# Kernel optimization log

Measured on AMD Instinct MI355X. Metric: run time of the kernel, lower is better.

Reference implementation:

```python
import jax, jax.numpy as jnp
import numpy as np

B, T, N, F_IN, F_OUT = 8, 64, 256, 128, 64
NEG_INF = -9e15


def setup_inputs() -> dict:
    key = jax.random.key(0)
    k_h, k_w, k_a, k_adj = jax.random.split(key, 4)
    h = jax.random.normal(k_h, (B, T, N, F_IN), dtype=jnp.float32)
    W = jax.random.normal(k_w, (F_IN, F_OUT), dtype=jnp.float32) * (1.414 / np.sqrt(F_IN))
    a = jax.random.normal(k_a, (2 * F_OUT, 1), dtype=jnp.float32) * 0.1
    # binary adjacency with guaranteed self-loops so every softmax row is valid
    adj = (jax.random.uniform(k_adj, (N, N)) > 0.5).astype(jnp.float32)
    adj = jnp.maximum(adj, jnp.eye(N, dtype=jnp.float32))
    return {"h": h, "W": W, "a": a, "adj": adj}


def reference(h, W, a, adj):
    # Wh: [B, T, N, F_OUT]
    Wh = jnp.einsum('btnf,fo->btno', h, W)
    a1 = a[:F_OUT, 0]   # [F_OUT]
    a2 = a[F_OUT:, 0]   # [F_OUT]
    Wh1 = jnp.einsum('btno,o->btn', Wh, a1)  # source scores
    Wh2 = jnp.einsum('btno,o->btn', Wh, a2)  # target scores
    # e: [B, T, N, N] = leakyrelu(Wh1_i + Wh2_j)
    e = jax.nn.leaky_relu(Wh1[..., :, None] + Wh2[..., None, :], negative_slope=0.01)
    attention = jnp.where(adj > 0, e, NEG_INF)
    alpha = jax.nn.softmax(attention, axis=-1)
    # dropout is identity at inference (training=False)
    h_prime = jnp.einsum('btnm,btmo->btno', alpha, Wh)
    return jax.nn.elu(h_prime)  # concat=True path
```

## Files before the change

### kernel.cpp

```cpp
#include <hip/hip_runtime.h>
#include <hip/hip_bf16.h>

#define NN 256
#define FI 128
#define FO 64
#define LOG2E 1.4426950408889634f

typedef short s16x8 __attribute__((ext_vector_type(8)));
typedef float f32x4 __attribute__((ext_vector_type(4)));

__device__ __forceinline__ unsigned f2bf1(float x) {
  union { float f; unsigned u; } v; v.f = x;
  unsigned r = v.u + 0x7FFFu + ((v.u >> 16) & 1u);
  return r >> 16;
}
__device__ __forceinline__ unsigned pack2(float a, float b) {
  return f2bf1(a) | (f2bf1(b) << 16);
}
__device__ __forceinline__ unsigned pktrunc(float lo, float hi) {
  union { float f; unsigned u; } a, b; a.f = hi; b.f = lo;
  return __builtin_amdgcn_perm(a.u, b.u, 0x07060302u);
}
__device__ __forceinline__ float fexp2(float x) {
#if __has_builtin(__builtin_amdgcn_exp2f)
  return __builtin_amdgcn_exp2f(x);
#else
  return exp2f(x);
#endif
}

__global__ __launch_bounds__(256) void gat_k0(const float* __restrict__ adj,
                                              unsigned* __restrict__ msk) {
  const int row = blockIdx.x;
  const int wv = threadIdx.x >> 6, lane = threadIdx.x & 63;
  float v = adj[row * NN + wv * 64 + lane];
  unsigned long long b = __ballot(v > 0.f);
  if (lane == 0) {
    msk[row * 8 + wv * 2]     = (unsigned)b;
    msk[row * 8 + wv * 2 + 1] = (unsigned)(b >> 32);
  }
}

struct K1Out { unsigned short* wB; float* wh1; float* wh2; };

__device__ __forceinline__ void k1_subtile(
    const float4 (&x)[4][2], int rw, int m, int q,
    const unsigned short* sWT, const float* sA, int bt, K1Out o_)
{
  s16x8 af[4];
  #pragma unroll
  for (int kt = 0; kt < 4; ++kt) {
    union { unsigned u[4]; s16x8 v; } pk;
    pk.u[0] = pack2(x[kt][0].x, x[kt][0].y);
    pk.u[1] = pack2(x[kt][0].z, x[kt][0].w);
    pk.u[2] = pack2(x[kt][1].x, x[kt][1].y);
    pk.u[3] = pack2(x[kt][1].z, x[kt][1].w);
    af[kt] = pk.v;
  }
  f32x4 acc[4];
  #pragma unroll
  for (int nt = 0; nt < 4; ++nt) acc[nt] = (f32x4){0.f, 0.f, 0.f, 0.f};
  #pragma unroll
  for (int kt = 0; kt < 4; ++kt)
    #pragma unroll
    for (int nt = 0; nt < 4; ++nt) {
      s16x8 bf = *(const s16x8*)&sWT[(16 * nt + m) * 136 + kt * 32 + q * 8];
      acc[nt] = __builtin_amdgcn_mfma_f32_16x16x32_bf16(af[kt], bf, acc[nt], 0, 0, 0);
    }

  {
    float p1[4] = {0.f,0.f,0.f,0.f}, p2[4] = {0.f,0.f,0.f,0.f};
    #pragma unroll
    for (int nt = 0; nt < 4; ++nt) {
      float a1v = sA[16 * nt + m];
      float a2v = sA[FO + 16 * nt + m];
      #pragma unroll
      for (int r = 0; r < 4; ++r) { p1[r] += acc[nt][r] * a1v; p2[r] += acc[nt][r] * a2v; }
    }
    #pragma unroll
    for (int off = 1; off < 16; off <<= 1)
      #pragma unroll
      for (int r = 0; r < 4; ++r) {
        p1[r] += __shfl_xor(p1[r], off);
        p2[r] += __shfl_xor(p2[r], off);
      }
    if (m == 0) {
      *(float4*)&o_.wh1[bt * NN + rw + 4 * q] =
          make_float4(p1[0]*LOG2E, p1[1]*LOG2E, p1[2]*LOG2E, p1[3]*LOG2E);
      *(float4*)&o_.wh2[bt * NN + rw + 4 * q] =
          make_float4(p2[0]*LOG2E, p2[1]*LOG2E, p2[2]*LOG2E, p2[3]*LOG2E);
    }
  }
  {
    int t  = (rw >> 3) + (q >> 1);
    int eo = (q & 1) * 4;
    #pragma unroll
    for (int nt = 0; nt < 4; ++nt) {
      int o = 16 * nt + m;
      int c = t ^ (o & 7);
      uint2 wrv;
      wrv.x = pack2(acc[nt][0], acc[nt][1]);
      wrv.y = pack2(acc[nt][2], acc[nt][3]);
      *(uint2*)&o_.wB[o * NN + c * 8 + eo] = wrv;
    }
  }
}

__global__ __launch_bounds__(256, 4) void gat_k1(
    const float* __restrict__ h, const float* __restrict__ W,
    const float* __restrict__ a,
    unsigned short* __restrict__ whT, float* __restrict__ wh1,
    float* __restrict__ wh2)
{
  const int bt   = blockIdx.x & 511;
  const int tile = blockIdx.x >> 9;
  const int tid  = threadIdx.x;
  const int lane = tid & 63;
  const int wv   = tid >> 6;
  const int m    = lane & 15;
  const int q    = lane >> 4;
  const int rw0  = tile * 128 + wv * 32;

  __shared__ __align__(16) unsigned short sWT[64 * 136];
  __shared__ __align__(16) float sA[2 * FO];

  const float* __restrict__ hB = h + (size_t)bt * NN * FI;

  float4 x0[4][2], x1[4][2];
  #pragma unroll
  for (int kt = 0; kt < 4; ++kt) {
    const float* p = hB + (size_t)(rw0 + m) * FI + kt * 32 + q * 8;
    x0[kt][0] = *(const float4*)p; x0[kt][1] = *(const float4*)(p + 4);
  }
  #pragma unroll
  for (int kt = 0; kt < 4; ++kt) {
    const float* p = hB + (size_t)(rw0 + 16 + m) * FI + kt * 32 + q * 8;
    x1[kt][0] = *(const float4*)p; x1[kt][1] = *(const float4*)(p + 4);
  }

  if (tid < 2 * FO) sA[tid] = a[tid];
  for (int idx = tid; idx < FI * FO; idx += 256) {
    int k = idx >> 6, o = idx & 63;
    sWT[o * 136 + k] = (unsigned short)f2bf1(W[idx]);
  }
  __syncthreads();

  K1Out o_{ whT + (size_t)bt * (FO * NN), wh1, wh2 };
  k1_subtile(x0, rw0,      m, q, sWT, sA, bt, o_);
  k1_subtile(x1, rw0 + 16, m, q, sWT, sA, bt, o_);
}

__global__ __launch_bounds__(256, 4) void gat_k2(
    const unsigned* __restrict__ msk,
    const unsigned short* __restrict__ whT,
    const float* __restrict__ wh1, const float* __restrict__ wh2,
    float* __restrict__ out)
{
  const int bt   = blockIdx.x & 511;
  const int tile = blockIdx.x >> 9;
  const int tid  = threadIdx.x;
  const int lane = tid & 63;
  const int wv   = tid >> 6;
  const int m    = lane & 15;
  const int q    = lane >> 4;

  __shared__ __align__(16) unsigned short sWhB[64 * 256];
  __shared__ __align__(16) float sW2[4][256];

  const unsigned short* wg = whT + (size_t)bt * (FO * NN);
  #pragma unroll
  for (int i = 0; i < 8; ++i) {
    const unsigned short* gp = wg + (size_t)(i * 256 + tid) * 8;
    unsigned short* lp = &sWhB[(i * 256 + wv * 64) * 8];
    __builtin_amdgcn_global_load_lds(
        (const __attribute__((address_space(1))) unsigned int*)gp,
        (__attribute__((address_space(3))) unsigned int*)lp, 16, 0, 0);
  }

  {
    float4 w2 = *(const float4*)&wh2[bt * NN + 4 * lane];
    *(float4*)&sW2[wv][4 * lane] = w2;
  }

  const int rw  = tile * 64 + wv * 16;
  const int row = rw + m;
  const float w1 = wh1[bt * NN + row];

  const uint4 mka = *(const uint4*)&msk[row * 8];
  const uint4 mkb = *(const uint4*)&msk[row * 8 + 4];
  const unsigned mkw[8] = {mka.x, mka.y, mka.z, mka.w, mkb.x, mkb.y, mkb.z, mkb.w};

  s16x8 A[8];
  float sum = 0.f;
  #pragma unroll
  for (int kt = 0; kt < 8; ++kt) {
    int j0 = kt * 32 + q * 8;
    float4 w20 = *(const float4*)&sW2[wv][j0];
    float4 w21 = *(const float4*)&sW2[wv][j0 + 4];
    unsigned wq = mkw[kt] >> (q * 8);
    float p[8];
    const float w2e[8] = {w20.x, w20.y, w20.z, w20.w, w21.x, w21.y, w21.z, w21.w};
    #pragma unroll
    for (int e = 0; e < 8; ++e) {
      float l = w1 + w2e[e];
      l = fmaxf(l, 0.01f * l);
      union { float f; int i; } u_; u_.f = fexp2(l);
      u_.i &= ((int)(wq << (31 - e))) >> 31;
      p[e] = u_.f;
      sum += u_.f;
    }
    union { unsigned u[4]; s16x8 v; } pk;
    pk.u[0] = pktrunc(p[0], p[1]);
    pk.u[1] = pktrunc(p[2], p[3]);
    pk.u[2] = pktrunc(p[4], p[5]);
    pk.u[3] = pktrunc(p[6], p[7]);
    A[kt] = pk.v;
  }
  sum += __shfl_xor(sum, 16);
  sum += __shfl_xor(sum, 32);
  const float inv = __builtin_amdgcn_rcpf(sum);

  __syncthreads();

  f32x4 acc[4];
  #pragma unroll
  for (int nt = 0; nt < 4; ++nt) acc[nt] = (f32x4){0.f, 0.f, 0.f, 0.f};
  #pragma unroll
  for (int kt = 0; kt < 8; ++kt) {
    int t = kt * 4 + q;
    #pragma unroll
    for (int nt = 0; nt < 4; ++nt) {
      int o = 16 * nt + m;
      s16x8 bf = *(const s16x8*)&sWhB[o * NN + ((t ^ (o & 7)) * 8)];
      acc[nt] = __builtin_amdgcn_mfma_f32_16x16x32_bf16(A[kt], bf, acc[nt], 0, 0, 0);
    }
  }

  float invr[4];
  #pragma unroll
  for (int r = 0; r < 4; ++r) invr[r] = __shfl(inv, 4 * q + r);
  float* outB = out + (size_t)bt * NN * FO;
  #pragma unroll
  for (int nt = 0; nt < 4; ++nt) {
    int col = 16 * nt + m;
    #pragma unroll
    for (int r = 0; r < 4; ++r) {
      int orow = rw + 4 * q + r;
      float v = acc[nt][r] * invr[r];
      float ev = fexp2(v * LOG2E) - 1.f;
      v = v > 0.f ? v : ev;
      outB[orow * FO + col] = v;
    }
  }
}

extern "C" void kernel_launch(void* const* d_in, const int* in_sizes, int n_in,
                              void* d_out, int out_size, void* d_ws, size_t ws_size,
                              hipStream_t stream) {
  const float* h   = (const float*)d_in[0];
  const float* W   = (const float*)d_in[1];
  const float* a   = (const float*)d_in[2];
  const float* adj = (const float*)d_in[3];
  float* out = (float*)d_out;

  unsigned short* whT = (unsigned short*)d_ws;
  float* wh1 = (float*)((char*)d_ws + (size_t)512 * FO * NN * 2);
  float* wh2 = wh1 + (size_t)512 * NN;
  unsigned* msk = (unsigned*)(wh2 + (size_t)512 * NN);

  gat_k0<<<dim3(256),  dim3(256), 0, stream>>>(adj, msk);
  gat_k1<<<dim3(1024), dim3(256), 0, stream>>>(h, W, a, whT, wh1, wh2);
  gat_k2<<<dim3(2048), dim3(256), 0, stream>>>(msk, whT, wh1, wh2, out);
}
```

Measured before the change: 141.4 us.

## Fuse projection and attention kernels into one per-batch block using LDS

Merges the Wh projection kernel and the attention/aggregation kernel into one kernel with one 512-thread block per (b,t). Wh (in bf16), Wh1 and Wh2 now stay in shared memory under a new swizzled chunk layout, so they are never written to or read back from global memory, and one launch goes away. The cost is fewer blocks (512 instead of 2048), each doing more serial work, and about 52 KB of LDS per block, which reduces occupancy and the overlap between blocks. The W conversion to bf16 is also done only once per (b,t) instead of once per tile.

```diff
diff --git a/kernel.cpp b/kernel.cpp
--- a/kernel.cpp
+++ b/kernel.cpp
@@ -41,12 +41,12 @@
   }
 }
 
-struct K1Out { unsigned short* wB; float* wh1; float* wh2; };
-
-__device__ __forceinline__ void k1_subtile(
-    const float4 (&x)[4][2], int rw, int m, int q,
-    const unsigned short* sWT, const float* sA, int bt, K1Out o_)
+__device__ __forceinline__ void phaseA_sub(
+    const float4 (&x)[4][2], int w, int s, int m, int q,
+    const unsigned short* sWT, const float* sA,
+    unsigned short* sWhB, float* sWh1, float* sWh2)
 {
+  const int R = 32 * w + 16 * s;
   s16x8 af[4];
   #pragma unroll
   for (int kt = 0; kt < 4; ++kt) {
@@ -85,171 +85,139 @@
         p2[r] += __shfl_xor(p2[r], off);
       }
     if (m == 0) {
-      *(float4*)&o_.wh1[bt * NN + rw + 4 * q] =
+      *(float4*)&sWh1[R + 4 * q] =
           make_float4(p1[0]*LOG2E, p1[1]*LOG2E, p1[2]*LOG2E, p1[3]*LOG2E);
-      *(float4*)&o_.wh2[bt * NN + rw + 4 * q] =
+      *(float4*)&sWh2[R + 4 * q] =
           make_float4(p2[0]*LOG2E, p2[1]*LOG2E, p2[2]*LOG2E, p2[3]*LOG2E);
     }
   }
   {
-    int t  = (rw >> 3) + (q >> 1);
-    int eo = (q & 1) * 4;
-    #pragma unroll
-    for (int nt = 0; nt < 4; ++nt) {
-      int o = 16 * nt + m;
-      int c = t ^ (o & 7);
+    const int qB = (2 * s + (q >> 1)) & 3;
+    #pragma unroll
+    for (int nt = 0; nt < 4; ++nt) {
+      int chunk = ((w * 4 + nt) * 16 + m) * 4 + (qB ^ (m & 3));
       uint2 wrv;
       wrv.x = pack2(acc[nt][0], acc[nt][1]);
       wrv.y = pack2(acc[nt][2], acc[nt][3]);
-      *(uint2*)&o_.wB[o * NN + c * 8 + eo] = wrv;
-    }
-  }
-}
-
-__global__ __launch_bounds__(256, 4) void gat_k1(
+      *(uint2*)((char*)sWhB + chunk * 16 + (q & 1) * 8) = wrv;
+    }
+  }
+}
+
+__global__ __launch_bounds__(512, 4) void gat_fused(
     const float* __restrict__ h, const float* __restrict__ W,
-    const float* __restrict__ a,
-    unsigned short* __restrict__ whT, float* __restrict__ wh1,
-    float* __restrict__ wh2)
+    const float* __restrict__ a, const unsigned* __restrict__ msk,
+    float* __restrict__ out)
 {
-  const int bt   = blockIdx.x & 511;
-  const int tile = blockIdx.x >> 9;
+  const int bt   = blockIdx.x;
   const int tid  = threadIdx.x;
   const int lane = tid & 63;
-  const int wv   = tid >> 6;
+  const int w    = tid >> 6;
   const int m    = lane & 15;
   const int q    = lane >> 4;
-  const int rw0  = tile * 128 + wv * 32;
-
+
+  __shared__ __align__(16) unsigned short sWhB[64 * 256];
   __shared__ __align__(16) unsigned short sWT[64 * 136];
+  __shared__ __align__(16) float sWh1[NN], sWh2[NN];
   __shared__ __align__(16) float sA[2 * FO];
 
   const float* __restrict__ hB = h + (size_t)bt * NN * FI;
 
-  float4 x0[4][2], x1[4][2];
+  float4 x0[4][2];
   #pragma unroll
   for (int kt = 0; kt < 4; ++kt) {
-    const float* p = hB + (size_t)(rw0 + m) * FI + kt * 32 + q * 8;
-    x0[kt][0] = *(const float4*)p; x0[kt][1] = *(const float4*)(p + 4);
-  }
-  #pragma unroll
-  for (int kt = 0; kt < 4; ++kt) {
-    const float* p = hB + (size_t)(rw0 + 16 + m) * FI + kt * 32 + q * 8;
-    x1[kt][0] = *(const float4*)p; x1[kt][1] = *(const float4*)(p + 4);
+    const float* p = hB + (size_t)(32 * w + m) * FI + kt * 32 + q * 8;
+    x0[kt][0] = *(const float4*)p;
+    x0[kt][1] = *(const float4*)(p + 4);
   }
 
   if (tid < 2 * FO) sA[tid] = a[tid];
-  for (int idx = tid; idx < FI * FO; idx += 256) {
+  for (int idx = tid; idx < FI * FO; idx += 512) {
     int k = idx >> 6, o = idx & 63;
     sWT[o * 136 + k] = (unsigned short)f2bf1(W[idx]);
   }
   __syncthreads();
 
-  K1Out o_{ whT + (size_t)bt * (FO * NN), wh1, wh2 };
-  k1_subtile(x0, rw0,      m, q, sWT, sA, bt, o_);
-  k1_subtile(x1, rw0 + 16, m, q, sWT, sA, bt, o_);
-}
-
-__global__ __launch_bounds__(256, 4) void gat_k2(
-    const unsigned* __restrict__ msk,
-    const unsigned short* __restrict__ whT,
-    const float* __restrict__ wh1, const float* __restrict__ wh2,
-    float* __restrict__ out)
-{
-  const int bt   = blockIdx.x & 511;
-  const int tile = blockIdx.x >> 9;
-  const int tid  = threadIdx.x;
-  const int lane = tid & 63;
-  const int wv   = tid >> 6;
-  const int m    = lane & 15;
-  const int q    = lane >> 4;
-
-  __shared__ __align__(16) unsigned short sWhB[64 * 256];
-  __shared__ __align__(16) float sW2[4][256];
-
-  const unsigned short* wg = whT + (size_t)bt * (FO * NN);
-  #pragma unroll
-  for (int i = 0; i < 8; ++i) {
-    const unsigned short* gp = wg + (size_t)(i * 256 + tid) * 8;
-    unsigned short* lp = &sWhB[(i * 256 + wv * 64) * 8];
-    __builtin_amdgcn_global_load_lds(
-        (const __attribute__((address_space(1))) unsigned int*)gp,
-        (__attribute__((address_space(3))) unsigned int*)lp, 16, 0, 0);
-  }
-
-  {
-    float4 w2 = *(const float4*)&wh2[bt * NN + 4 * lane];
-    *(float4*)&sW2[wv][4 * lane] = w2;
-  }
-
-  const int rw  = tile * 64 + wv * 16;
-  const int row = rw + m;
-  const float w1 = wh1[bt * NN + row];
-
-  const uint4 mka = *(const uint4*)&msk[row * 8];
-  const uint4 mkb = *(const uint4*)&msk[row * 8 + 4];
-  const unsigned mkw[8] = {mka.x, mka.y, mka.z, mka.w, mkb.x, mkb.y, mkb.z, mkb.w};
-
-  s16x8 A[8];
-  float sum = 0.f;
-  #pragma unroll
-  for (int kt = 0; kt < 8; ++kt) {
-    int j0 = kt * 32 + q * 8;
-    float4 w20 = *(const float4*)&sW2[wv][j0];
-    float4 w21 = *(const float4*)&sW2[wv][j0 + 4];
-    unsigned wq = mkw[kt] >> (q * 8);
-    float p[8];
-    const float w2e[8] = {w20.x, w20.y, w20.z, w20.w, w21.x, w21.y, w21.z, w21.w};
-    #pragma unroll
-    for (int e = 0; e < 8; ++e) {
-      float l = w1 + w2e[e];
-      l = fmaxf(l, 0.01f * l);
-      union { float f; int i; } u_; u_.f = fexp2(l);
-      u_.i &= ((int)(wq << (31 - e))) >> 31;
-      p[e] = u_.f;
-      sum += u_.f;
-    }
-    union { unsigned u[4]; s16x8 v; } pk;
-    pk.u[0] = pktrunc(p[0], p[1]);
-    pk.u[1] = pktrunc(p[2], p[3]);
-    pk.u[2] = pktrunc(p[4], p[5]);
-    pk.u[3] = pktrunc(p[6], p[7]);
-    A[kt] = pk.v;
-  }
-  sum += __shfl_xor(sum, 16);
-  sum += __shfl_xor(sum, 32);
-  const float inv = __builtin_amdgcn_rcpf(sum);
-
+  float4 x1[4][2];
+  #pragma unroll
+  for (int kt = 0; kt < 4; ++kt) {
+    const float* p = hB + (size_t)(32 * w + 16 + m) * FI + kt * 32 + q * 8;
+    x1[kt][0] = *(const float4*)p;
+    x1[kt][1] = *(const float4*)(p + 4);
+  }
+
+  phaseA_sub(x0, w, 0, m, q, sWT, sA, sWhB, sWh1, sWh2);
+  phaseA_sub(x1, w, 1, m, q, sWT, sA, sWhB, sWh1, sWh2);
   __syncthreads();
 
-  f32x4 acc[4];
-  #pragma unroll
-  for (int nt = 0; nt < 4; ++nt) acc[nt] = (f32x4){0.f, 0.f, 0.f, 0.f};
-  #pragma unroll
-  for (int kt = 0; kt < 8; ++kt) {
-    int t = kt * 4 + q;
-    #pragma unroll
-    for (int nt = 0; nt < 4; ++nt) {
-      int o = 16 * nt + m;
-      s16x8 bf = *(const s16x8*)&sWhB[o * NN + ((t ^ (o & 7)) * 8)];
-      acc[nt] = __builtin_amdgcn_mfma_f32_16x16x32_bf16(A[kt], bf, acc[nt], 0, 0, 0);
-    }
-  }
-
-  float invr[4];
-  #pragma unroll
-  for (int r = 0; r < 4; ++r) invr[r] = __shfl(inv, 4 * q + r);
   float* outB = out + (size_t)bt * NN * FO;
   #pragma unroll
-  for (int nt = 0; nt < 4; ++nt) {
-    int col = 16 * nt + m;
-    #pragma unroll
-    for (int r = 0; r < 4; ++r) {
-      int orow = rw + 4 * q + r;
-      float v = acc[nt][r] * invr[r];
-      float ev = fexp2(v * LOG2E) - 1.f;
-      v = v > 0.f ? v : ev;
-      outB[orow * FO + col] = v;
+  for (int t = 0; t < 2; ++t) {
+    const int R2  = 32 * w + 16 * t;
+    const int row = R2 + m;
+
+    const uint4 mka = *(const uint4*)&msk[row * 8];
+    const uint4 mkb = *(const uint4*)&msk[row * 8 + 4];
+    const unsigned mkw[8] = {mka.x, mka.y, mka.z, mka.w, mkb.x, mkb.y, mkb.z, mkb.w};
+    const float w1 = sWh1[row];
+
+    s16x8 A[8];
+    float sum = 0.f;
+    #pragma unroll
+    for (int kt = 0; kt < 8; ++kt) {
+      int j0 = kt * 32 + q * 8;
+      float4 w20 = *(const float4*)&sWh2[j0];
+      float4 w21 = *(const float4*)&sWh2[j0 + 4];
+      unsigned wq = mkw[kt] >> (q * 8);
+      float p[8];
+      const float w2e[8] = {w20.x, w20.y, w20.z, w20.w, w21.x, w21.y, w21.z, w21.w};
+      #pragma unroll
+      for (int e = 0; e < 8; ++e) {
+        float l = w1 + w2e[e];
+        l = fmaxf(l, 0.01f * l);
+        union { float f; int i; } u_; u_.f = fexp2(l);
+        u_.i &= ((int)(wq << (31 - e))) >> 31;
+        p[e] = u_.f;
+        sum += u_.f;
+      }
+      union { unsigned u[4]; s16x8 v; } pk;
+      pk.u[0] = pktrunc(p[0], p[1]);
+      pk.u[1] = pktrunc(p[2], p[3]);
+      pk.u[2] = pktrunc(p[4], p[5]);
+      pk.u[3] = pktrunc(p[6], p[7]);
+      A[kt] = pk.v;
+    }
+    sum += __shfl_xor(sum, 16);
+    sum += __shfl_xor(sum, 32);
+    const float inv = __builtin_amdgcn_rcpf(sum);
+
+    f32x4 acc[4];
+    #pragma unroll
+    for (int nt = 0; nt < 4; ++nt) acc[nt] = (f32x4){0.f, 0.f, 0.f, 0.f};
+    #pragma unroll
+    for (int kt = 0; kt < 8; ++kt) {
+      #pragma unroll
+      for (int nt = 0; nt < 4; ++nt) {
+        int chunk = ((kt * 4 + nt) * 16 + m) * 4 + (q ^ (m & 3));
+        s16x8 bf = *(const s16x8*)&sWhB[chunk * 8];
+        acc[nt] = __builtin_amdgcn_mfma_f32_16x16x32_bf16(A[kt], bf, acc[nt], 0, 0, 0);
+      }
+    }
+
+    float invr[4];
+    #pragma unroll
+    for (int r = 0; r < 4; ++r) invr[r] = __shfl(inv, 4 * q + r);
+    #pragma unroll
+    for (int nt = 0; nt < 4; ++nt) {
+      int col = 16 * nt + m;
+      #pragma unroll
+      for (int r = 0; r < 4; ++r) {
+        int orow = R2 + 4 * q + r;
+        float v = acc[nt][r] * invr[r];
+        float ev = fexp2(v * LOG2E) - 1.f;
+        v = v > 0.f ? v : ev;
+        outB[orow * FO + col] = v;
+      }
     }
   }
 }
@@ -263,12 +231,8 @@
   const float* adj = (const float*)d_in[3];
   float* out = (float*)d_out;
 
-  unsigned short* whT = (unsigned short*)d_ws;
-  float* wh1 = (float*)((char*)d_ws + (size_t)512 * FO * NN * 2);
-  float* wh2 = wh1 + (size_t)512 * NN;
-  unsigned* msk = (unsigned*)(wh2 + (size_t)512 * NN);
-
-  gat_k0<<<dim3(256),  dim3(256), 0, stream>>>(adj, msk);
-  gat_k1<<<dim3(1024), dim3(256), 0, stream>>>(h, W, a, whT, wh1, wh2);
-  gat_k2<<<dim3(2048), dim3(256), 0, stream>>>(msk, whT, wh1, wh2, out);
-}
+  unsigned* msk = (unsigned*)d_ws;
+
+  gat_k0<<<dim3(256), dim3(256), 0, stream>>>(adj, msk);
+  gat_fused<<<dim3(512), dim3(512), 0, stream>>>(h, W, a, msk, out);
+}
```

Measured after the change: 151.8 us. 7.4% more time.
